# Kernel optimization log

Hardware: AMD Instinct MI355X
Metric: run time of the kernel (lower is better)

Reference implementation:

```python
import jax, jax.numpy as jnp
import numpy as np
from jax import lax

IN_CH = 512
OUT_CH = 512
KERNEL = 3
STYLE_DIM = 512
BATCH = 8
HW = 64
EPS = 1e-08
LR_MUL = 1.0


def setup_inputs() -> dict:
    key = jax.random.key(0)
    k1, k2, k3, k4 = jax.random.split(key, 4)
    x = jax.random.normal(k1, (BATCH, IN_CH, HW, HW), dtype=jnp.float32)
    style = jax.random.normal(k2, (BATCH, STYLE_DIM), dtype=jnp.float32)
    weight = jax.random.normal(k3, (1, OUT_CH, IN_CH, KERNEL, KERNEL), dtype=jnp.float32)
    mod_weight = jax.random.normal(k4, (IN_CH, STYLE_DIM), dtype=jnp.float32)
    mod_bias = jnp.ones((IN_CH,), dtype=jnp.float32)  # bias_init=1
    return {"x": x, "style": style, "weight": weight,
            "mod_weight": mod_weight, "mod_bias": mod_bias}


def reference(x, style, weight, mod_weight, mod_bias):
    batch, in_ch, h, w_dim = x.shape
    conv_scale = 1.0 / np.sqrt(in_ch * KERNEL * KERNEL)
    lin_scale = 1.0 / np.sqrt(STYLE_DIM) * LR_MUL

    # EqualizedLinear modulation: style -> per-channel scale, shape (B, in_ch)
    s = style @ (mod_weight * lin_scale).T + mod_bias * LR_MUL

    # Modulate: (B, out, in, k, k)
    w = conv_scale * weight * s[:, None, :, None, None]
    # Demodulate
    demod = lax.rsqrt(jnp.sum(w * w, axis=(2, 3, 4)) + EPS)  # (B, out)
    w = w * demod[:, :, None, None, None]

    pad = KERNEL // 2

    def conv_one(xi, wi):
        # xi: (in, H, W), wi: (out, in, k, k)
        return lax.conv_general_dilated(
            xi[None], wi, window_strides=(1, 1),
            padding=[(pad, pad), (pad, pad)],
            dimension_numbers=("NCHW", "OIHW", "NCHW"))[0]

    out = jax.vmap(conv_one)(x, w)  # (B, out, H, W)
    return out
```

## Files before the change

kernel.cpp:

```cpp
#include <hip/hip_runtime.h>
#include <hip/hip_bf16.h>
#include <cstdint>

#define IN_CH 512
#define OUT_CH 512
#define STYLE_DIM 512
#define BATCH 8
#define HW 64

typedef __bf16 bf16x8 __attribute__((ext_vector_type(8)));
typedef float f32x16 __attribute__((ext_vector_type(16)));

__device__ __forceinline__ void gload_lds16(const void* g, void* l) {
  __builtin_amdgcn_global_load_lds(
      (const __attribute__((address_space(1))) unsigned int*)g,
      (__attribute__((address_space(3))) unsigned int*)l,
      16, 0, 0);
}

#define WAITV(N) asm volatile("s_waitcnt vmcnt(" #N ")" ::: "memory")
#define BARRIER() do { asm volatile("" ::: "memory"); __builtin_amdgcn_s_barrier(); \
                       asm volatile("" ::: "memory"); } while (0)

__global__ void k_style(const float* __restrict__ style, const float* __restrict__ modw,
                        const float* __restrict__ modb, float* __restrict__ s_out) {
  __shared__ float st[BATCH * STYLE_DIM];
  const int tid = threadIdx.x;
  for (int i = tid; i < BATCH * STYLE_DIM; i += 256) st[i] = style[i];
  __syncthreads();
  const int ic = blockIdx.x * 4 + (tid >> 6);
  const int l = tid & 63;
  const float* mr = modw + (size_t)ic * STYLE_DIM + l * 8;
  float m[8];
  #pragma unroll
  for (int j = 0; j < 8; ++j) m[j] = mr[j];
  float accs[8];
  #pragma unroll
  for (int b = 0; b < 8; ++b) {
    const float* sb = st + b * STYLE_DIM + l * 8;
    float a = 0.f;
    #pragma unroll
    for (int j = 0; j < 8; ++j) a += m[j] * sb[j];
    accs[b] = a;
  }
  #pragma unroll
  for (int off = 32; off; off >>= 1) {
    #pragma unroll
    for (int b = 0; b < 8; ++b) accs[b] += __shfl_down(accs[b], off, 64);
  }
  if (l == 0) {
    #pragma unroll
    for (int b = 0; b < 8; ++b)
      s_out[b * IN_CH + ic] = accs[b] * 0.04419417382415922f + modb[ic];
  }
}

__global__ void k_wprep(const float* __restrict__ w, float* __restrict__ wsq,
                        __bf16* __restrict__ wb) {
  const int idx = blockIdx.x * 256 + threadIdx.x;
  const int oc = idx >> 9, ic = idx & 511;
  const float* p = w + ((size_t)oc * IN_CH + ic) * 9;
  const int icw = ic ^ ((oc & 7) << 3);
  float sum = 0.f;
  #pragma unroll
  for (int t = 0; t < 9; ++t) {
    float v = p[t];
    sum += v * v;
    wb[((size_t)(t * OUT_CH) + oc) * IN_CH + icw] = (__bf16)v;
  }
  wsq[oc * IN_CH + ic] = sum;
}

__global__ void k_demod(const float* __restrict__ s, const float* __restrict__ wsq,
                        float* __restrict__ scale) {
  const int oc = blockIdx.x;
  const int l = threadIdx.x;
  const float* wr = wsq + (size_t)oc * IN_CH + l * 8;
  float w8[8];
  #pragma unroll
  for (int j = 0; j < 8; ++j) w8[j] = wr[j];
  #pragma unroll
  for (int b = 0; b < 8; ++b) {
    const float* sb = s + b * IN_CH + l * 8;
    float acc = 0.f;
    #pragma unroll
    for (int j = 0; j < 8; ++j) { float sv = sb[j]; acc += sv * sv * w8[j]; }
    #pragma unroll
    for (int off = 32; off; off >>= 1) acc += __shfl_down(acc, off, 64);
    if (l == 0)
      scale[b * OUT_CH + oc] =
          rsqrtf(acc * (1.0f / 4608.0f) + 1e-8f) * 0.014731391274719732f;
  }
}

__global__ void k_xprep(const float* __restrict__ x, const float* __restrict__ s,
                        __bf16* __restrict__ xg) {
  const int b = blockIdx.x >> 6, y = blockIdx.x & 63;
  const int w = threadIdx.x >> 6, lane = threadIdx.x & 63;
  const float* sr = s + b * IN_CH;
  #pragma unroll
  for (int it = 0; it < 8; ++it) {
    const int ug = it * 8 + w;
    bf16x8 pk;
    #pragma unroll
    for (int j = 0; j < 8; ++j) {
      const int ic = ug * 8 + j;
      pk[j] = (__bf16)(x[(((size_t)(b * IN_CH) + ic) * HW + y) * HW + lane] * sr[ic]);
    }
    *(bf16x8*)(xg + ((((size_t)(b * 64 + ug) * HW + y) * HW + lane) * 8)) = pk;
  }
}

__global__ __launch_bounds__(256, 1) void k_conv(
    const __bf16* __restrict__ Wg,
    const __bf16* __restrict__ Xg,
    const float* __restrict__ scale,
    float* __restrict__ out)
{
  __shared__ __attribute__((aligned(16))) __bf16 Xs[6 * 66 * 64];
  __shared__ __attribute__((aligned(16))) __bf16 Wl[3][256 * 64];
  __shared__ __attribute__((aligned(16))) __bf16 Dump[2048];

  const int tid = threadIdx.x;
  const int lane = tid & 63;
  const int wv = tid >> 6;
  const int wm = wv >> 1;
  const int wn = wv & 1;
  const int ln31 = lane & 31;
  const int laneK = lane >> 5;

  const int bid0 = blockIdx.x;
  const int bid = (bid0 & 7) * 32 + (bid0 >> 3);
  const int octile = bid & 1;
  const int ptile = (bid >> 1) & 15;
  const int b = bid >> 5;
  const int oc0 = octile * 256;
  const int r0 = ptile * 4;

  auto stage_w = [&](int chunk, int tap, int bsel) {
    const int ic0 = chunk * 64;
    #pragma unroll
    for (int i = 0; i < 8; ++i) {
      const int sidx = tid + 256 * i;
      const int oc = sidx >> 3, u = sidx & 7;
      gload_lds16(Wg + (((size_t)(tap * OUT_CH) + oc0 + oc) * IN_CH + ic0 + u * 8),
                  &Wl[bsel][oc * 64 + u * 8]);
    }
  };
  auto stage_x = [&](int chunk) {
    #pragma unroll
    for (int j = 0; j < 12; ++j) {
      const int row = j >> 1;
      const int col = (j & 1) * 32 + (tid >> 3);
      const int u = tid & 7;
      const int y = r0 - 1 + row;
      const bool ok = (y >= 0 && y < HW);
      const int yc = ok ? y : (y < 0 ? 0 : HW - 1);
      const int ug = chunk * 8 + (u ^ ((col + 1) & 7));
      void* dst = ok ? (void*)&Xs[(row * 66 + col + 1) * 64 + u * 8]
                     : (void*)&Dump[((tid & 63) * 8) | ((tid >> 6) << 9)];
      gload_lds16(Xg + ((((size_t)(b * 64 + ug) * HW + yc) * HW + col) * 8), dst);
    }
  };

  {
    float4 z = {0.f, 0.f, 0.f, 0.f};
    float4* p = (float4*)Xs;
    for (int i = tid; i < 6 * 66 * 64 / 8; i += 256) p[i] = z;
  }
  __syncthreads();
  stage_x(0);
  stage_w(0, 0, 0);
  stage_w(0, 1, 1);
  WAITV(8);
  BARRIER();

  f32x16 acc[4][4] = {};
  const int akey8 = (ln31 & 7) << 3;
  const int kb = laneK * 8;

  int tap = 0, chunk = 0, buf = 0;

  for (int s = 0; s < 72; ++s) {
    if (s + 2 < 72) {
      int t2 = tap + 2, c2 = chunk, b2 = buf + 2;
      if (t2 >= 9) { t2 -= 9; ++c2; }
      if (b2 >= 3) b2 -= 3;
      stage_w(c2, t2, b2);
    }
    if (s == 70)                 { WAITV(8); }
    else if (s == 71)            { WAITV(0); }
    else if (tap == 0 && s > 0)  { WAITV(8); }
    else                         { WAITV(16); }
    BARRIER();

    const int dy = tap / 3 - 1, dx = tap % 3 - 1;
    const int col0 = ln31 + 1 + dx;
    const int bkey8 = (col0 & 7) << 3;
    const __bf16* __restrict__ wbase = &Wl[buf][(wm * 128 + ln31) * 64];
    const __bf16* xb[4];
    #pragma unroll
    for (int nf = 0; nf < 4; ++nf)
      xb[nf] = &Xs[((wn * 2 + (nf >> 1) + 1 + dy) * 66 + (nf & 1) * 32 + col0) * 64];

    #pragma unroll
    for (int ks = 0; ks < 4; ++ks) {
      const int ael = (ks * 16 + kb) ^ akey8;
      const int bel = (ks * 16 + kb) ^ bkey8;
      bf16x8 av[4], bv[4];
      #pragma unroll
      for (int mf = 0; mf < 4; ++mf) av[mf] = *(const bf16x8*)(wbase + mf * 2048 + ael);
      #pragma unroll
      for (int nf = 0; nf < 4; ++nf) bv[nf] = *(const bf16x8*)(xb[nf] + bel);
      #pragma unroll
      for (int mf = 0; mf < 4; ++mf) {
        #pragma unroll
        for (int nf = 0; nf < 4; ++nf)
          acc[mf][nf] = __builtin_amdgcn_mfma_f32_32x32x16_bf16(av[mf], bv[nf], acc[mf][nf], 0, 0, 0);
      }
    }
    BARRIER();

    if (tap == 8 && chunk < 7) stage_x(chunk + 1);

    if (++tap == 9) { tap = 0; ++chunk; }
    if (++buf == 3) buf = 0;
  }

  const int y0 = r0 + wn * 2;
  #pragma unroll
  for (int mf = 0; mf < 4; ++mf) {
    #pragma unroll
    for (int reg = 0; reg < 16; ++reg) {
      const int rowid = (reg & 3) + 8 * (reg >> 2) + 4 * laneK;
      const int oc = oc0 + wm * 128 + mf * 32 + rowid;
      const float sc = scale[b * OUT_CH + oc];
      float* obase = out + (size_t)(b * OUT_CH + oc) * (HW * HW);
      #pragma unroll
      for (int nf = 0; nf < 4; ++nf)
        obase[(y0 + (nf >> 1)) * HW + (nf & 1) * 32 + ln31] = acc[mf][nf][reg] * sc;
    }
  }
}

extern "C" void kernel_launch(void* const* d_in, const int* in_sizes, int n_in,
                              void* d_out, int out_size, void* d_ws, size_t ws_size,
                              hipStream_t stream) {
  const float* x      = (const float*)d_in[0];
  const float* style  = (const float*)d_in[1];
  const float* weight = (const float*)d_in[2];
  const float* modw   = (const float*)d_in[3];
  const float* modb   = (const float*)d_in[4];
  float* out = (float*)d_out;

  char* ws = (char*)d_ws;
  float*  s_buf = (float*)(ws + 0);
  float*  scale = (float*)(ws + 16384);
  float*  wsq   = (float*)(ws + 32768);
  __bf16* wb    = (__bf16*)(ws + 32768 + 1048576);
  __bf16* xg    = (__bf16*)(ws + 32768 + 1048576 + 9 * OUT_CH * IN_CH * 2);

  k_style<<<128, 256, 0, stream>>>(style, modw, modb, s_buf);
  k_wprep<<<1024, 256, 0, stream>>>(weight, wsq, wb);
  k_demod<<<512, 64, 0, stream>>>(s_buf, wsq, scale);
  k_xprep<<<BATCH * HW, 512, 0, stream>>>(x, s_buf, xg);
  k_conv<<<256, 256, 0, stream>>>(wb, xg, scale, out);
}
```

Before: 183.9 us.

## Use 8 waves per conv block with register double-buffered LDS fragment prefetch

Raises the conv block from 4 to 8 waves, so each wave covers one output row with half as many accumulators. The main loop is restructured to split each k-step into two MFMA phases. The next tap's A fragments are prefetched from LDS into alternating register sets while the current MFMAs run, with s_setprio around the MFMA phases. Global-to-LDS staging and the vmcnt waits are retuned to match. The goal is more latency hiding and better overlap of LDS reads with matrix math, at the cost of more barrier coordination and register pressure under launch_bounds(512,2).

```diff
diff --git a/kernel.cpp b/kernel.cpp
--- a/kernel.cpp
+++ b/kernel.cpp
@@ -19,6 +19,7 @@
 }
 
 #define WAITV(N) asm volatile("s_waitcnt vmcnt(" #N ")" ::: "memory")
+#define LGKM0()  asm volatile("s_waitcnt lgkmcnt(0)" ::: "memory")
 #define BARRIER() do { asm volatile("" ::: "memory"); __builtin_amdgcn_s_barrier(); \
                        asm volatile("" ::: "memory"); } while (0)
 
@@ -111,7 +112,7 @@
   }
 }
 
-__global__ __launch_bounds__(256, 1) void k_conv(
+__global__ __launch_bounds__(512, 2) void k_conv(
     const __bf16* __restrict__ Wg,
     const __bf16* __restrict__ Xg,
     const float* __restrict__ scale,
@@ -123,9 +124,9 @@
 
   const int tid = threadIdx.x;
   const int lane = tid & 63;
-  const int wv = tid >> 6;
-  const int wm = wv >> 1;
-  const int wn = wv & 1;
+  const int wid = tid >> 6;
+  const int wm = wid >> 2;
+  const int wn = wid & 3;
   const int ln31 = lane & 31;
   const int laneK = lane >> 5;
 
@@ -137,28 +138,27 @@
   const int oc0 = octile * 256;
   const int r0 = ptile * 4;
 
-  auto stage_w = [&](int chunk, int tap, int bsel) {
-    const int ic0 = chunk * 64;
-    #pragma unroll
-    for (int i = 0; i < 8; ++i) {
-      const int sidx = tid + 256 * i;
+  auto stage_w = [&](int chunkv, int tapv, int bsel) {
+    const int ic0 = chunkv * 64;
+    #pragma unroll
+    for (int i = 0; i < 4; ++i) {
+      const int sidx = tid + 512 * i;
       const int oc = sidx >> 3, u = sidx & 7;
-      gload_lds16(Wg + (((size_t)(tap * OUT_CH) + oc0 + oc) * IN_CH + ic0 + u * 8),
+      gload_lds16(Wg + (((size_t)(tapv * OUT_CH) + oc0 + oc) * IN_CH + ic0 + u * 8),
                   &Wl[bsel][oc * 64 + u * 8]);
     }
   };
-  auto stage_x = [&](int chunk) {
-    #pragma unroll
-    for (int j = 0; j < 12; ++j) {
-      const int row = j >> 1;
-      const int col = (j & 1) * 32 + (tid >> 3);
+  auto stage_x = [&](int chunkv) {
+    #pragma unroll
+    for (int j = 0; j < 6; ++j) {
+      const int col = tid >> 3;
       const int u = tid & 7;
-      const int y = r0 - 1 + row;
+      const int y = r0 - 1 + j;
       const bool ok = (y >= 0 && y < HW);
-      const int yc = ok ? y : (y < 0 ? 0 : HW - 1);
-      const int ug = chunk * 8 + (u ^ ((col + 1) & 7));
-      void* dst = ok ? (void*)&Xs[(row * 66 + col + 1) * 64 + u * 8]
-                     : (void*)&Dump[((tid & 63) * 8) | ((tid >> 6) << 9)];
+      const int yc = ok ? y : 0;
+      const int ug = chunkv * 8 + (u ^ ((col + 1) & 7));
+      void* dst = ok ? (void*)&Xs[(j * 66 + col + 1) * 64 + u * 8]
+                     : (void*)&Dump[(tid & 255) * 8];
       gload_lds16(Xg + ((((size_t)(b * 64 + ug) * HW + yc) * HW + col) * 8), dst);
     }
   };
@@ -166,79 +166,106 @@
   {
     float4 z = {0.f, 0.f, 0.f, 0.f};
     float4* p = (float4*)Xs;
-    for (int i = tid; i < 6 * 66 * 64 / 8; i += 256) p[i] = z;
+    for (int i = tid; i < 6 * 66 * 64 / 8; i += 512) p[i] = z;
   }
   __syncthreads();
   stage_x(0);
   stage_w(0, 0, 0);
   stage_w(0, 1, 1);
-  WAITV(8);
+  WAITV(4);
   BARRIER();
 
-  f32x16 acc[4][4] = {};
+  f32x16 acc[4][2] = {};
   const int akey8 = (ln31 & 7) << 3;
   const int kb = laneK * 8;
 
-  int tap = 0, chunk = 0, buf = 0;
-
-  for (int s = 0; s < 72; ++s) {
-    if (s + 2 < 72) {
-      int t2 = tap + 2, c2 = chunk, b2 = buf + 2;
-      if (t2 >= 9) { t2 -= 9; ++c2; }
-      if (b2 >= 3) b2 -= 3;
-      stage_w(c2, t2, b2);
-    }
-    if (s == 70)                 { WAITV(8); }
-    else if (s == 71)            { WAITV(0); }
-    else if (tap == 0 && s > 0)  { WAITV(8); }
-    else                         { WAITV(16); }
-    BARRIER();
-
-    const int dy = tap / 3 - 1, dx = tap % 3 - 1;
-    const int col0 = ln31 + 1 + dx;
-    const int bkey8 = (col0 & 7) << 3;
-    const __bf16* __restrict__ wbase = &Wl[buf][(wm * 128 + ln31) * 64];
-    const __bf16* xb[4];
-    #pragma unroll
-    for (int nf = 0; nf < 4; ++nf)
-      xb[nf] = &Xs[((wn * 2 + (nf >> 1) + 1 + dy) * 66 + (nf & 1) * 32 + col0) * 64];
-
-    #pragma unroll
-    for (int ks = 0; ks < 4; ++ks) {
-      const int ael = (ks * 16 + kb) ^ akey8;
-      const int bel = (ks * 16 + kb) ^ bkey8;
-      bf16x8 av[4], bv[4];
-      #pragma unroll
-      for (int mf = 0; mf < 4; ++mf) av[mf] = *(const bf16x8*)(wbase + mf * 2048 + ael);
-      #pragma unroll
-      for (int nf = 0; nf < 4; ++nf) bv[nf] = *(const bf16x8*)(xb[nf] + bel);
-      #pragma unroll
-      for (int mf = 0; mf < 4; ++mf) {
-        #pragma unroll
-        for (int nf = 0; nf < 4; ++nf)
-          acc[mf][nf] = __builtin_amdgcn_mfma_f32_32x32x16_bf16(av[mf], bv[nf], acc[mf][nf], 0, 0, 0);
-      }
-    }
-    BARRIER();
-
-    if (tap == 8 && chunk < 7) stage_x(chunk + 1);
-
-    if (++tap == 9) { tap = 0; ++chunk; }
-    if (++buf == 3) buf = 0;
-  }
-
-  const int y0 = r0 + wn * 2;
+  bf16x8 A0[2][4], A1[2][4];
+  bf16x8 aB[2][4];
+  bf16x8 vA[2][2], vB[2][2];
+
+#define LOAD_AV(P, Aa, WB)                                                   \
+  { _Pragma("unroll") for (int kk = 0; kk < 2; ++kk) {                       \
+      const int ae = (((kk + (P)) * 16 + kb) ^ akey8);                       \
+      _Pragma("unroll") for (int mf = 0; mf < 4; ++mf)                       \
+        Aa[kk][mf] = *(const bf16x8*)((WB) + mf * 2048 + ae);                \
+    } }
+#define LOAD_BV(P, Vv, XB, BK)                                               \
+  { _Pragma("unroll") for (int kk = 0; kk < 2; ++kk) {                       \
+      const int be = (((kk + (P)) * 16 + kb) ^ (BK));                        \
+      Vv[kk][0] = *(const bf16x8*)((XB) + be);                               \
+      Vv[kk][1] = *(const bf16x8*)((XB) + 2048 + be);                        \
+    } }
+#define MFMA_PHASE(Aa, Vv)                                                   \
+  { _Pragma("unroll") for (int kk = 0; kk < 2; ++kk)                         \
+    _Pragma("unroll") for (int mf = 0; mf < 4; ++mf) {                       \
+      acc[mf][0] = __builtin_amdgcn_mfma_f32_32x32x16_bf16(Aa[kk][mf], Vv[kk][0], acc[mf][0], 0, 0, 0); \
+      acc[mf][1] = __builtin_amdgcn_mfma_f32_32x32x16_bf16(Aa[kk][mf], Vv[kk][1], acc[mf][1], 0, 0, 0); \
+    } }
+
+  {
+    const __bf16* wbase = &Wl[0][(wm * 128 + ln31) * 64];
+    LOAD_AV(0, A0, wbase)
+  }
+
+  int tap = 0, chunk = 0, buf = 0, s = 0;
+
+#define ITER(CA, NA)                                                          \
+  {                                                                           \
+    const int dy = tap / 3 - 1, dx = tap % 3 - 1;                             \
+    const int col0 = ln31 + 1 + dx;                                           \
+    const int bkey8 = (col0 & 7) << 3;                                        \
+    const __bf16* wbase = &Wl[buf][(wm * 128 + ln31) * 64];                   \
+    const __bf16* xb0 = &Xs[((wn + 1 + dy) * 66 + col0) * 64];                \
+    if (tap == 0 && s > 0) {          \
+      WAITV(0); BARRIER();                                                    \
+      LOAD_AV(0, CA, wbase)                                                   \
+    }                                                                         \
+    LOAD_BV(0, vA, xb0, bkey8)                                                \
+    LOAD_BV(2, vB, xb0, bkey8)                                                \
+    LOAD_AV(2, aB, wbase)                                                     \
+    __builtin_amdgcn_s_setprio(1);                                            \
+    MFMA_PHASE(CA, vA)                                                        \
+    __builtin_amdgcn_s_setprio(0);                                            \
+    if (s + 2 < 72) {                                                         \
+      int t2 = tap + 2, c2 = chunk;                                           \
+      if (t2 >= 9) { t2 -= 9; ++c2; }                                         \
+      const int b2 = (buf + 2 >= 3) ? buf - 1 : buf + 2;                      \
+      stage_w(c2, t2, b2);                                                    \
+    }                                                                         \
+    if (s >= 70) { WAITV(0); } else { WAITV(4); }                             \
+    if (tap == 8 && chunk < 7) { LGKM0(); }         \
+    BARRIER();                                                                \
+    if (tap != 8) {                     \
+      const int bufn = (buf == 2) ? 0 : buf + 1;                              \
+      const __bf16* wbase2 = &Wl[bufn][(wm * 128 + ln31) * 64];               \
+      LOAD_AV(0, NA, wbase2)                                                  \
+    }                                                                         \
+    __builtin_amdgcn_s_setprio(1);                                            \
+    MFMA_PHASE(aB, vB)                                                        \
+    __builtin_amdgcn_s_setprio(0);                                            \
+    if (tap == 8 && chunk < 7) stage_x(chunk + 1);                            \
+    if (++tap == 9) { tap = 0; ++chunk; }                                     \
+    buf = (buf == 2) ? 0 : buf + 1;                                           \
+    ++s;                                                                      \
+  }
+
+  #pragma unroll 1
+  for (int it = 0; it < 36; ++it) {
+    ITER(A0, A1)
+    ITER(A1, A0)
+  }
+
+  const int y = r0 + wn;
   #pragma unroll
   for (int mf = 0; mf < 4; ++mf) {
     #pragma unroll
     for (int reg = 0; reg < 16; ++reg) {
       const int rowid = (reg & 3) + 8 * (reg >> 2) + 4 * laneK;
-      const int oc = oc0 + wm * 128 + mf * 32 + rowid;
+      const int oc = oc0 + 128 * wm + 32 * mf + rowid;
       const float sc = scale[b * OUT_CH + oc];
-      float* obase = out + (size_t)(b * OUT_CH + oc) * (HW * HW);
-      #pragma unroll
-      for (int nf = 0; nf < 4; ++nf)
-        obase[(y0 + (nf >> 1)) * HW + (nf & 1) * 32 + ln31] = acc[mf][nf][reg] * sc;
+      float* op = out + (((size_t)(b * OUT_CH + oc) * HW + y) * HW) + ln31;
+      op[0] = acc[mf][0][reg] * sc;
+      op[32] = acc[mf][1][reg] * sc;
     }
   }
 }
@@ -264,5 +291,5 @@
   k_wprep<<<1024, 256, 0, stream>>>(weight, wsq, wb);
   k_demod<<<512, 64, 0, stream>>>(s_buf, wsq, scale);
   k_xprep<<<BATCH * HW, 512, 0, stream>>>(x, s_buf, xg);
-  k_conv<<<256, 256, 0, stream>>>(wb, xg, scale, out);
-}
+  k_conv<<<256, 512, 0, stream>>>(wb, xg, scale, out);
+}
```

Result: slower. 321.0 us (+74.5%).

## Halve conv tile and K-chunk to fit two blocks per CU

Applied to the files above, without the earlier changes.

The conv kernel tile shrinks from 4 output rows to 2 and the K chunk from 64 to 32 input channels. LDS drops from triple- to double-buffered weights and the accumulators are halved, which lets two blocks run per CU over a grid of 512 instead of 256. The weight swizzle is changed to match the narrower rows, and s_setprio is added around the MFMA bursts. The cost is twice as many pipeline steps and barriers, less reuse per LDS load, and a shallower prefetch of one step.

```diff
diff --git a/kernel.cpp b/kernel.cpp
--- a/kernel.cpp
+++ b/kernel.cpp
@@ -60,7 +60,7 @@
   const int idx = blockIdx.x * 256 + threadIdx.x;
   const int oc = idx >> 9, ic = idx & 511;
   const float* p = w + ((size_t)oc * IN_CH + ic) * 9;
-  const int icw = ic ^ ((oc & 7) << 3);
+  const int icw = ic ^ ((oc & 3) << 3);
   float sum = 0.f;
   #pragma unroll
   for (int t = 0; t < 9; ++t) {
@@ -111,15 +111,15 @@
   }
 }
 
-__global__ __launch_bounds__(256, 1) void k_conv(
+__global__ __launch_bounds__(256, 2) void k_conv(
     const __bf16* __restrict__ Wg,
     const __bf16* __restrict__ Xg,
     const float* __restrict__ scale,
     float* __restrict__ out)
 {
-  __shared__ __attribute__((aligned(16))) __bf16 Xs[6 * 66 * 64];
-  __shared__ __attribute__((aligned(16))) __bf16 Wl[3][256 * 64];
-  __shared__ __attribute__((aligned(16))) __bf16 Dump[2048];
+  __shared__ __attribute__((aligned(16))) __bf16 Xs[4 * 66 * 32];
+  __shared__ __attribute__((aligned(16))) __bf16 Wl[2][256 * 32];
+  __shared__ __attribute__((aligned(16))) __bf16 Dump[512];
 
   const int tid = threadIdx.x;
   const int lane = tid & 63;
@@ -130,35 +130,33 @@
   const int laneK = lane >> 5;
 
   const int bid0 = blockIdx.x;
-  const int bid = (bid0 & 7) * 32 + (bid0 >> 3);
+  const int bid = (bid0 & 7) * 64 + (bid0 >> 3);
   const int octile = bid & 1;
-  const int ptile = (bid >> 1) & 15;
-  const int b = bid >> 5;
+  const int ptile = (bid >> 1) & 31;
+  const int b = bid >> 6;
   const int oc0 = octile * 256;
-  const int r0 = ptile * 4;
-
-  auto stage_w = [&](int chunk, int tap, int bsel) {
-    const int ic0 = chunk * 64;
-    #pragma unroll
-    for (int i = 0; i < 8; ++i) {
+  const int r0 = ptile * 2;
+
+  auto stage_w = [&](int chunkv, int tapv, int bsel) {
+    #pragma unroll
+    for (int i = 0; i < 4; ++i) {
       const int sidx = tid + 256 * i;
-      const int oc = sidx >> 3, u = sidx & 7;
-      gload_lds16(Wg + (((size_t)(tap * OUT_CH) + oc0 + oc) * IN_CH + ic0 + u * 8),
-                  &Wl[bsel][oc * 64 + u * 8]);
+      const int oc = sidx >> 2, u = sidx & 3;
+      gload_lds16(Wg + (((size_t)(tapv * OUT_CH) + oc0 + oc) * IN_CH + chunkv * 32 + u * 8),
+                  &Wl[bsel][oc * 32 + u * 8]);
     }
   };
-  auto stage_x = [&](int chunk) {
-    #pragma unroll
-    for (int j = 0; j < 12; ++j) {
-      const int row = j >> 1;
-      const int col = (j & 1) * 32 + (tid >> 3);
-      const int u = tid & 7;
+  auto stage_x = [&](int chunkv) {
+    const int col = tid >> 2;
+    const int u = tid & 3;
+    const int ug = chunkv * 4 + (u ^ ((col + 1) & 3));
+    #pragma unroll
+    for (int row = 0; row < 4; ++row) {
       const int y = r0 - 1 + row;
       const bool ok = (y >= 0 && y < HW);
-      const int yc = ok ? y : (y < 0 ? 0 : HW - 1);
-      const int ug = chunk * 8 + (u ^ ((col + 1) & 7));
-      void* dst = ok ? (void*)&Xs[(row * 66 + col + 1) * 64 + u * 8]
-                     : (void*)&Dump[((tid & 63) * 8) | ((tid >> 6) << 9)];
+      const int yc = ok ? y : 0;
+      void* dst = ok ? (void*)&Xs[(row * 66 + col + 1) * 32 + u * 8]
+                     : (void*)&Dump[(tid & 63) * 8];
       gload_lds16(Xg + ((((size_t)(b * 64 + ug) * HW + yc) * HW + col) * 8), dst);
     }
   };
@@ -166,68 +164,60 @@
   {
     float4 z = {0.f, 0.f, 0.f, 0.f};
     float4* p = (float4*)Xs;
-    for (int i = tid; i < 6 * 66 * 64 / 8; i += 256) p[i] = z;
+    for (int i = tid; i < 4 * 66 * 32 / 8; i += 256) p[i] = z;
   }
   __syncthreads();
   stage_x(0);
   stage_w(0, 0, 0);
-  stage_w(0, 1, 1);
-  WAITV(8);
+  WAITV(0);
   BARRIER();
 
-  f32x16 acc[4][4] = {};
-  const int akey8 = (ln31 & 7) << 3;
+  f32x16 acc[4][2] = {};
+  const int akey = (ln31 & 3) << 3;
   const int kb = laneK * 8;
 
-  int tap = 0, chunk = 0, buf = 0;
-
-  for (int s = 0; s < 72; ++s) {
-    if (s + 2 < 72) {
-      int t2 = tap + 2, c2 = chunk, b2 = buf + 2;
-      if (t2 >= 9) { t2 -= 9; ++c2; }
-      if (b2 >= 3) b2 -= 3;
-      stage_w(c2, t2, b2);
-    }
-    if (s == 70)                 { WAITV(8); }
-    else if (s == 71)            { WAITV(0); }
-    else if (tap == 0 && s > 0)  { WAITV(8); }
-    else                         { WAITV(16); }
+  int tap = 0, chunk = 0;
+
+  for (int s = 0; s < 144; ++s) {
+    if (s + 1 < 144) {
+      int t1 = tap + 1, c1 = chunk;
+      if (t1 == 9) { t1 = 0; ++c1; }
+      stage_w(c1, t1, (s + 1) & 1);
+    }
+    if (s == 143) { WAITV(0); } else { WAITV(4); }
     BARRIER();
 
     const int dy = tap / 3 - 1, dx = tap % 3 - 1;
     const int col0 = ln31 + 1 + dx;
-    const int bkey8 = (col0 & 7) << 3;
-    const __bf16* __restrict__ wbase = &Wl[buf][(wm * 128 + ln31) * 64];
-    const __bf16* xb[4];
-    #pragma unroll
-    for (int nf = 0; nf < 4; ++nf)
-      xb[nf] = &Xs[((wn * 2 + (nf >> 1) + 1 + dy) * 66 + (nf & 1) * 32 + col0) * 64];
-
-    #pragma unroll
-    for (int ks = 0; ks < 4; ++ks) {
-      const int ael = (ks * 16 + kb) ^ akey8;
-      const int bel = (ks * 16 + kb) ^ bkey8;
-      bf16x8 av[4], bv[4];
+    const int bkey = (col0 & 3) << 3;
+    const __bf16* __restrict__ wbase = &Wl[s & 1][(wm * 128 + ln31) * 32];
+    const __bf16* __restrict__ xb0 = &Xs[((wn + 1 + dy) * 66 + col0) * 32];
+
+    #pragma unroll
+    for (int ks = 0; ks < 2; ++ks) {
+      const int ael = (ks * 16 + kb) ^ akey;
+      const int bel = (ks * 16 + kb) ^ bkey;
+      bf16x8 av[4], bv[2];
       #pragma unroll
-      for (int mf = 0; mf < 4; ++mf) av[mf] = *(const bf16x8*)(wbase + mf * 2048 + ael);
-      #pragma unroll
-      for (int nf = 0; nf < 4; ++nf) bv[nf] = *(const bf16x8*)(xb[nf] + bel);
+      for (int mf = 0; mf < 4; ++mf) av[mf] = *(const bf16x8*)(wbase + mf * 1024 + ael);
+      bv[0] = *(const bf16x8*)(xb0 + bel);
+      bv[1] = *(const bf16x8*)(xb0 + 32 * 32 + bel);
+      __builtin_amdgcn_s_setprio(1);
       #pragma unroll
       for (int mf = 0; mf < 4; ++mf) {
-        #pragma unroll
-        for (int nf = 0; nf < 4; ++nf)
-          acc[mf][nf] = __builtin_amdgcn_mfma_f32_32x32x16_bf16(av[mf], bv[nf], acc[mf][nf], 0, 0, 0);
+        acc[mf][0] = __builtin_amdgcn_mfma_f32_32x32x16_bf16(av[mf], bv[0], acc[mf][0], 0, 0, 0);
+        acc[mf][1] = __builtin_amdgcn_mfma_f32_32x32x16_bf16(av[mf], bv[1], acc[mf][1], 0, 0, 0);
       }
+      __builtin_amdgcn_s_setprio(0);
     }
     BARRIER();
 
-    if (tap == 8 && chunk < 7) stage_x(chunk + 1);
+    if (tap == 8 && chunk < 15) stage_x(chunk + 1);
 
     if (++tap == 9) { tap = 0; ++chunk; }
-    if (++buf == 3) buf = 0;
-  }
-
-  const int y0 = r0 + wn * 2;
+  }
+
+  const int y = r0 + wn;
   #pragma unroll
   for (int mf = 0; mf < 4; ++mf) {
     #pragma unroll
@@ -235,10 +225,9 @@
       const int rowid = (reg & 3) + 8 * (reg >> 2) + 4 * laneK;
       const int oc = oc0 + wm * 128 + mf * 32 + rowid;
       const float sc = scale[b * OUT_CH + oc];
-      float* obase = out + (size_t)(b * OUT_CH + oc) * (HW * HW);
-      #pragma unroll
-      for (int nf = 0; nf < 4; ++nf)
-        obase[(y0 + (nf >> 1)) * HW + (nf & 1) * 32 + ln31] = acc[mf][nf][reg] * sc;
+      float* op = out + (((size_t)(b * OUT_CH + oc) * HW + y) * HW) + ln31;
+      op[0] = acc[mf][0][reg] * sc;
+      op[32] = acc[mf][1][reg] * sc;
     }
   }
 }
@@ -264,5 +253,5 @@
   k_wprep<<<1024, 256, 0, stream>>>(weight, wsq, wb);
   k_demod<<<512, 64, 0, stream>>>(s_buf, wsq, scale);
   k_xprep<<<BATCH * HW, 512, 0, stream>>>(x, s_buf, xg);
-  k_conv<<<256, 256, 0, stream>>>(wb, xg, scale, out);
-}
+  k_conv<<<512, 256, 0, stream>>>(wb, xg, scale, out);
+}
```

Result: slower. 209.6 us (+14.0%).
